# Kernel tuning notes

Hardware: AMD Instinct MI355X
Metric: run time of the kernel (lower is better)

Reference implementation:

```python
import jax, jax.numpy as jnp
import numpy as np

D_MODEL = 2048
N_HEADS = 16
HEAD_DIM = D_MODEL // N_HEADS
LN_EPS = 1e-6  # flax.linen.LayerNorm default
NEG_INF = float('-inf')


def _layernorm_scale_only(x, scale):
    # flax LayerNorm with use_bias=False: normalize over last axis, scale only
    mean = jnp.mean(x, axis=-1, keepdims=True)
    var = jnp.var(x, axis=-1, keepdims=True)
    return (x - mean) * jax.lax.rsqrt(var + LN_EPS) * scale


def setup_inputs() -> dict:
    key = jax.random.key(0)
    ks = jax.random.split(key, 4)
    B, S = 2, 2048
    x = jax.random.normal(ks[0], (B, S, D_MODEL), dtype=jnp.float32)
    Wqkv = jax.random.normal(ks[1], (D_MODEL, 3 * D_MODEL), dtype=jnp.float32) * 0.02
    q_ln_scale = jnp.ones((D_MODEL,), dtype=jnp.float32)
    k_ln_scale = jnp.ones((D_MODEL,), dtype=jnp.float32)
    out_W = jax.random.normal(ks[2], (D_MODEL, D_MODEL), dtype=jnp.float32) * 0.02
    return {"x": x, "Wqkv": Wqkv, "q_ln_scale": q_ln_scale,
            "k_ln_scale": k_ln_scale, "out_W": out_W}


def reference(x, Wqkv, q_ln_scale, k_ln_scale, out_W):
    B, S, _ = x.shape
    qkv = jnp.einsum('bsd,de->bse', x, Wqkv)  # [B,S,3*D] (no bias)
    q, k, v = jnp.split(qkv, 3, axis=-1)
    # QK LayerNorm (attn_qk_ln=True, no bias)
    q = _layernorm_scale_only(q, q_ln_scale)
    k = _layernorm_scale_only(k, k_ln_scale)
    # split heads: [B,S,H,Dh]
    q = q.reshape(B, S, N_HEADS, HEAD_DIM)
    k = k.reshape(B, S, N_HEADS, HEAD_DIM)
    v = v.reshape(B, S, N_HEADS, HEAD_DIM)
    # scaled scores [B,H,S,S]
    scores = jnp.einsum('bshd,bthd->bhst', q / jnp.sqrt(jnp.float32(HEAD_DIM)), k)
    # causal mask: triu(ones, k=1) marks strictly-future positions -> -inf
    causal = jnp.triu(jnp.ones((S, S), dtype=bool), 1)
    scores = jnp.where(causal, NEG_INF, scores)
    # kv-cache mask: arange(S) < S - past_position - S = 0 -> all False (no-op
    # with past_position=0 and no layer_past), faithfully omitted.
    attn = jax.nn.softmax(scores, axis=-1)
    ctx = jnp.einsum('bhst,bthd->bshd', attn, v)  # [B,S,H,Dh]
    out = jnp.einsum('bsd,de->bse', ctx.reshape(B, S, D_MODEL), out_W)
    return out
```

## Files before the change

kernel.cpp:

```cpp
#include <hip/hip_runtime.h>


typedef float f32x4 __attribute__((ext_vector_type(4)));
typedef short s16x8 __attribute__((ext_vector_type(8)));
typedef short s16x4 __attribute__((ext_vector_type(4)));

static __device__ __forceinline__ unsigned short f2bf(float f) {
  unsigned u = __builtin_bit_cast(unsigned, f);
  unsigned r = u + 0x7fffu + ((u >> 16) & 1u);
  return (unsigned short)(r >> 16);
}
static __device__ __forceinline__ float bf2f(unsigned short s) {
  unsigned u = ((unsigned)s) << 16;
  return __builtin_bit_cast(float, u);
}

static __device__ __forceinline__ void gload_lds16(const unsigned short* g, unsigned short* l) {
  __builtin_amdgcn_global_load_lds((const __attribute__((address_space(1))) void*)g,
                                   (__attribute__((address_space(3))) void*)l, 16, 0, 0);
}

__global__ __launch_bounds__(256) void k_cvt4(const float4* __restrict__ in,
                                              s16x4* __restrict__ out, int n) {
  int i = blockIdx.x * 256 + threadIdx.x;
  if (i >= n) return;
  float4 v = in[i];
  s16x4 o = { (short)f2bf(v.x), (short)f2bf(v.y), (short)f2bf(v.z), (short)f2bf(v.w) };
  out[i] = o;
}

__global__ __launch_bounds__(256) void k_twT(const float* __restrict__ in,
                                             unsigned short* __restrict__ out,
                                             int K, int N) {
  __shared__ float tile[32][33];
  const int n0 = blockIdx.x * 32, k0 = blockIdx.y * 32;
  const int tx = threadIdx.x & 31, ty = threadIdx.x >> 5;
#pragma unroll
  for (int rr = 0; rr < 4; ++rr) {
    int kr = ty + rr * 8;
    tile[kr][tx] = in[(size_t)(k0 + kr) * N + n0 + tx];
  }
  __syncthreads();
#pragma unroll
  for (int rr = 0; rr < 4; ++rr) {
    int nr = ty + rr * 8;
    out[(size_t)(n0 + nr) * K + k0 + tx] = f2bf(tile[tx][nr]);
  }
}

template <int BF16OUT>
__global__ __launch_bounds__(512, 2) void k_g3b(const unsigned short* __restrict__ A,
                                                const unsigned short* __restrict__ Bt,
                                                void* __restrict__ Cout,
                                                int N, int K, int npx) {
  __shared__ unsigned short sA[3 * 128 * 64];
  __shared__ unsigned short sB[3 * 256 * 64];
  const int t = threadIdx.x;
  const int wid = t >> 6, lane = t & 63, g = lane >> 4, l15 = lane & 15;
  const int wm2 = wid >> 2, wn2 = wid & 3;
  const int xr = l15 & 7;

  const int xcd = (int)blockIdx.x & 7, idx = (int)blockIdx.x >> 3;
  const int m0 = (idx / npx) * 128;
  const int n0 = (xcd * npx + idx % npx) * 256;

  const int srow = t >> 3;
  const int sslot = (t & 7) ^ (srow & 7);
  const unsigned short* pA = A  + (size_t)(m0 + srow) * K + sslot * 8;
  const unsigned short* pB = Bt + (size_t)(n0 + srow) * K + sslot * 8;

  auto stage = [&](int kt, int buf) {
#pragma unroll
    for (int j = 0; j < 2; ++j)
      gload_lds16(pA + (size_t)(j * 64) * K + kt * 64,
                  sA + buf * 8192 + j * 4096 + t * 8);
#pragma unroll
    for (int j = 0; j < 4; ++j)
      gload_lds16(pB + (size_t)(j * 64) * K + kt * 64,
                  sB + buf * 16384 + j * 4096 + t * 8);
  };

  const int sl0 = (g ^ xr) * 8, sl1 = ((4 + g) ^ xr) * 8;
  const int arow = wm2 * 64 + l15;
  const int brow = wn2 * 32 + l15;

  f32x4 acc[2][4][2];
#pragma unroll
  for (int h = 0; h < 2; ++h)
#pragma unroll
    for (int fm = 0; fm < 4; ++fm)
#pragma unroll
      for (int fn = 0; fn < 2; ++fn) acc[h][fm][fn] = (f32x4){0.f, 0.f, 0.f, 0.f};

  const int NK = K >> 6;
  stage(0, 0);
  stage(1, 1);
  int b0 = 0, b1 = 1, b2 = 2;

  for (int s = 0; s < NK; ++s) {
    if (s + 2 < NK) stage(s + 2, b2);

    if (s + 2 < NK)      asm volatile("s_waitcnt vmcnt(12)" ::: "memory");
    else if (s + 1 < NK) asm volatile("s_waitcnt vmcnt(6)" ::: "memory");
    else                 asm volatile("s_waitcnt vmcnt(0)" ::: "memory");
    __builtin_amdgcn_sched_barrier(0);
    __builtin_amdgcn_s_barrier();
    __builtin_amdgcn_sched_barrier(0);

    const unsigned short* aT = sA + b0 * 8192;
    const unsigned short* bT = sB + b0 * 16384;
    s16x8 af[4][2], bfr[2][2][2];
#pragma unroll
    for (int fm = 0; fm < 4; ++fm) {
      af[fm][0] = *(const s16x8*)&aT[(arow + fm * 16) * 64 + sl0];
      af[fm][1] = *(const s16x8*)&aT[(arow + fm * 16) * 64 + sl1];
    }
#pragma unroll
    for (int h = 0; h < 2; ++h)
#pragma unroll
      for (int fn = 0; fn < 2; ++fn) {
        bfr[h][fn][0] = *(const s16x8*)&bT[(h * 128 + brow + fn * 16) * 64 + sl0];
        bfr[h][fn][1] = *(const s16x8*)&bT[(h * 128 + brow + fn * 16) * 64 + sl1];
      }

    __builtin_amdgcn_s_setprio(1);
#pragma unroll
    for (int fm = 0; fm < 4; ++fm)
#pragma unroll
      for (int h = 0; h < 2; ++h)
#pragma unroll
        for (int fn = 0; fn < 2; ++fn)
#pragma unroll
          for (int ks = 0; ks < 2; ++ks)
            acc[h][fm][fn] = __builtin_amdgcn_mfma_f32_16x16x32_bf16(
                af[fm][ks], bfr[h][fn][ks], acc[h][fm][fn], 0, 0, 0);
    __builtin_amdgcn_s_setprio(0);

    __builtin_amdgcn_sched_barrier(0);
    __builtin_amdgcn_s_barrier();

    int tmp = b0; b0 = b1; b1 = b2; b2 = tmp;
  }

#pragma unroll
  for (int h = 0; h < 2; ++h)
#pragma unroll
    for (int fm = 0; fm < 4; ++fm)
#pragma unroll
      for (int fn = 0; fn < 2; ++fn)
#pragma unroll
        for (int r = 0; r < 4; ++r) {
          const int row = m0 + wm2 * 64 + fm * 16 + g * 4 + r;
          const int col = n0 + h * 128 + wn2 * 32 + fn * 16 + l15;
          if (BF16OUT)
            ((unsigned short*)Cout)[(size_t)row * N + col] = f2bf(acc[h][fm][fn][r]);
          else
            ((float*)Cout)[(size_t)row * N + col] = acc[h][fm][fn][r];
        }
}

__global__ __launch_bounds__(256) void k_ln(unsigned short* __restrict__ qkv,
                                            const float* __restrict__ qsc,
                                            const float* __restrict__ ksc) {
  __shared__ float red[8];
  const int t = threadIdx.x;
  const int w = t >> 6;
  unsigned short* base = qkv + (size_t)blockIdx.x * 6144;
#pragma unroll
  for (int part = 0; part < 2; ++part) {
    unsigned short* p = base + part * 2048 + t * 8;
    s16x8 v = *(const s16x8*)p;
    float f[8], s = 0.f, q = 0.f;
#pragma unroll
    for (int j = 0; j < 8; j++) { f[j] = bf2f((unsigned short)v[j]); s += f[j]; q += f[j] * f[j]; }
#pragma unroll
    for (int m = 1; m < 64; m <<= 1) { s += __shfl_xor(s, m); q += __shfl_xor(q, m); }
    __syncthreads();
    if ((t & 63) == 0) { red[w] = s; red[4 + w] = q; }
    __syncthreads();
    s = red[0] + red[1] + red[2] + red[3];
    q = red[4] + red[5] + red[6] + red[7];
    float mean = s * (1.f / 2048.f);
    float var = q * (1.f / 2048.f) - mean * mean;
    float inv = rsqrtf(var + 1e-6f);
    const float* sc = part ? ksc : qsc;
    float extra = part ? 1.0f : 0.12751743f;
    s16x8 o;
#pragma unroll
    for (int j = 0; j < 8; j++) o[j] = (short)f2bf((f[j] - mean) * inv * (sc[t * 8 + j] * extra));
    *(s16x8*)p = o;
  }
}

__global__ __launch_bounds__(256) void k_vT(const unsigned short* __restrict__ qkv,
                                            unsigned short* __restrict__ vt) {
  __shared__ unsigned short tl[64][136];
  const int bh = blockIdx.y;
  const int b = bh >> 4, h = bh & 15;
  const int s0 = blockIdx.x * 64;
  const int t = threadIdx.x;
#pragma unroll
  for (int it = 0; it < 4; ++it) {
    int flat = it * 256 + t;
    int r = flat >> 4, c = flat & 15;
    s16x8 v = *(const s16x8*)(qkv + (size_t)(b * 2048 + s0 + r) * 6144 + 4096 + h * 128 + c * 8);
    *((s16x8*)&tl[r][c * 8]) = v;
  }
  __syncthreads();
#pragma unroll
  for (int it = 0; it < 4; ++it) {
    int flat = it * 256 + t;
    int d = flat >> 3, cs = flat & 7;
    s16x8 o;
#pragma unroll
    for (int e = 0; e < 8; e++) {
      int key = (cs >> 2) * 32 + (e >> 2) * 16 + (cs & 3) * 4 + (e & 3);
      o[e] = (short)tl[key][d];
    }
    *(s16x8*)(vt + (size_t)(bh * 128 + d) * 2048 + s0 + cs * 8) = o;
  }
}

__global__ __launch_bounds__(256) void k_attn(const unsigned short* __restrict__ qkv,
                                              const unsigned short* __restrict__ vt,
                                              unsigned short* __restrict__ ctx) {
  __shared__ unsigned short sK[2][64 * 128];
  __shared__ unsigned short sV[2][128 * 64];
  const int t = threadIdx.x;
  const int w = t >> 6, lane = t & 63, g = lane >> 4, l15 = lane & 15;
  const int pair = blockIdx.x, h = blockIdx.y, b = blockIdx.z;
  const int qt0 = 31 - pair, qt1 = pair;
  const int n0 = qt0 + 1;
  const int NT = 33;
  const unsigned short* kbase = qkv + (size_t)(b * 2048) * 6144 + 2048 + h * 128;
  const unsigned short* vbase = vt + (size_t)((b * 16 + h) * 128) * 2048;

  auto issue_kv = [&](int k0, int bufi) {
#pragma unroll
    for (int it2 = 0; it2 < 4; ++it2) {
      int flat = it2 * 256 + t;
      int r = flat >> 4, c = flat & 15;
      gload_lds16(kbase + (size_t)(k0 + r) * 6144 + ((c ^ (r & 15)) * 8),
                  (unsigned short*)&sK[bufi][(it2 * 256 + w * 64) * 8]);
    }
#pragma unroll
    for (int it2 = 0; it2 < 4; ++it2) {
      int flat = it2 * 256 + t;
      int d = flat >> 3, z = flat & 7;
      gload_lds16(vbase + (size_t)d * 2048 + k0 + ((z ^ (d & 7)) * 8),
                  (unsigned short*)&sV[bufi][(it2 * 256 + w * 64) * 8]);
    }
  };

  s16x8 bq[4];
  auto load_q = [&](int q0) {
#pragma unroll
    for (int ks = 0; ks < 4; ++ks)
      bq[ks] = *(const s16x8*)(qkv + (size_t)(b * 2048 + q0 + w * 16 + l15) * 6144 +
                               h * 128 + (ks * 4 + g) * 8);
  };

  f32x4 o[8];
  float mrun, lrun;
  auto reset_state = [&]() {
#pragma unroll
    for (int nd = 0; nd < 8; ++nd) o[nd] = (f32x4){0.f, 0.f, 0.f, 0.f};
    mrun = -INFINITY; lrun = 0.f;
  };
  auto write_o = [&](int q0) {
    float ivr[4];
#pragma unroll
    for (int r = 0; r < 4; ++r) ivr[r] = 1.0f / __shfl(lrun, 4 * g + r);
#pragma unroll
    for (int nd = 0; nd < 8; ++nd) {
      const int col = h * 128 + nd * 16 + l15;
#pragma unroll
      for (int r = 0; r < 4; ++r) {
        const int row = b * 2048 + q0 + w * 16 + 4 * g + r;
        ctx[(size_t)row * 2048 + col] = f2bf(o[nd][r] * ivr[r]);
      }
    }
  };

  reset_state();
  load_q(qt0 * 64);
  issue_kv(0, 0);
  int cur = 0;

  for (int it = 0; it < NT; ++it) {
    const int seg = (it < n0) ? 0 : 1;
    const int qt = seg ? qt1 : qt0;
    const int kt = seg ? it - n0 : it;

    if (it + 1 < NT) {
      const int kn = (it + 1 < n0) ? it + 1 : it + 1 - n0;
      issue_kv(kn * 64, cur ^ 1);
      asm volatile("s_waitcnt vmcnt(8)" ::: "memory");
    } else {
      asm volatile("s_waitcnt vmcnt(0)" ::: "memory");
    }
    __builtin_amdgcn_sched_barrier(0);
    __builtin_amdgcn_s_barrier();

    if (seg == 1 && kt == 0) {
      write_o(qt0 * 64);
      reset_state();
      load_q(qt1 * 64);
    }

    const unsigned short* sKc = &sK[cur][0];
    const unsigned short* sVc = &sV[cur][0];

    f32x4 st[4];
#pragma unroll
    for (int mi = 0; mi < 4; ++mi) st[mi] = (f32x4){0.f, 0.f, 0.f, 0.f};
#pragma unroll
    for (int mi = 0; mi < 4; ++mi) {
#pragma unroll
      for (int ks = 0; ks < 4; ++ks) {
        s16x8 ak = *(const s16x8*)&sKc[(mi * 16 + l15) * 128 + (((ks * 4 + g) ^ l15) * 8)];
        st[mi] = __builtin_amdgcn_mfma_f32_16x16x32_bf16(ak, bq[ks], st[mi], 0, 0, 0);
      }
    }

    if (kt == qt) {
      const int qloc = w * 16 + l15;
#pragma unroll
      for (int mi = 0; mi < 4; ++mi)
#pragma unroll
        for (int r = 0; r < 4; ++r)
          if (mi * 16 + 4 * g + r > qloc) st[mi][r] = -INFINITY;
    }

    float mt = -INFINITY;
#pragma unroll
    for (int mi = 0; mi < 4; ++mi)
#pragma unroll
      for (int r = 0; r < 4; ++r) mt = fmaxf(mt, st[mi][r]);
    mt = fmaxf(mt, __shfl_xor(mt, 16));
    mt = fmaxf(mt, __shfl_xor(mt, 32));

    if (!__all(mt <= mrun + 8.f)) {
      const float mnew = fmaxf(mrun, mt);
      const float alpha = exp2f(mrun - mnew);
      lrun *= alpha;
      float ar[4];
#pragma unroll
      for (int r = 0; r < 4; ++r) ar[r] = __shfl(alpha, 4 * g + r);
#pragma unroll
      for (int nd = 0; nd < 8; ++nd)
#pragma unroll
        for (int r = 0; r < 4; ++r) o[nd][r] *= ar[r];
      mrun = mnew;
    }

    float ls = 0.f;
#pragma unroll
    for (int mi = 0; mi < 4; ++mi)
#pragma unroll
      for (int r = 0; r < 4; ++r) {
        float pp = exp2f(st[mi][r] - mrun);
        st[mi][r] = pp;
        ls += pp;
      }
    ls += __shfl_xor(ls, 16);
    ls += __shfl_xor(ls, 32);
    lrun += ls;

    s16x8 pa01, pa23;
#pragma unroll
    for (int j = 0; j < 8; ++j) {
      pa01[j] = (short)f2bf(st[j >> 2][j & 3]);
      pa23[j] = (short)f2bf(st[2 + (j >> 2)][j & 3]);
    }

#pragma unroll
    for (int nd = 0; nd < 8; ++nd) {
      const int d = nd * 16 + l15;
      const int zs = d & 7;
      s16x8 bv0 = *(const s16x8*)&sVc[d * 64 + ((g ^ zs) * 8)];
      s16x8 bv1 = *(const s16x8*)&sVc[d * 64 + (((4 + g) ^ zs) * 8)];
      o[nd] = __builtin_amdgcn_mfma_f32_16x16x32_bf16(pa01, bv0, o[nd], 0, 0, 0);
      o[nd] = __builtin_amdgcn_mfma_f32_16x16x32_bf16(pa23, bv1, o[nd], 0, 0, 0);
    }

    __builtin_amdgcn_sched_barrier(0);
    __builtin_amdgcn_s_barrier();
    cur ^= 1;
  }
  write_o(qt1 * 64);
}

extern "C" void kernel_launch(void* const* d_in, const int* in_sizes, int n_in,
                              void* d_out, int out_size, void* d_ws, size_t ws_size,
                              hipStream_t stream) {
  (void)in_sizes; (void)n_in; (void)out_size; (void)ws_size;
  const float* x    = (const float*)d_in[0];
  const float* Wqkv = (const float*)d_in[1];
  const float* qsc  = (const float*)d_in[2];
  const float* ksc  = (const float*)d_in[3];
  const float* outW = (const float*)d_in[4];

  char* ws = (char*)d_ws;
  unsigned short* xb  = (unsigned short*)(ws);
  unsigned short* wT  = (unsigned short*)(ws + 16777216);
  unsigned short* owT = (unsigned short*)(ws + 41943040);
  unsigned short* qkv = (unsigned short*)(ws + 50331648);
  unsigned short* vt  = (unsigned short*)(ws + 100663296);
  unsigned short* ctx = xb;

  k_cvt4<<<8192, 256, 0, stream>>>((const float4*)x, (s16x4*)xb, 2097152);
  k_twT<<<dim3(192, 64), 256, 0, stream>>>(Wqkv, wT, 2048, 6144);
  k_twT<<<dim3(64, 64), 256, 0, stream>>>(outW, owT, 2048, 2048);
  k_g3b<1><<<768, 512, 0, stream>>>(xb, wT, qkv, 6144, 2048, 3);
  k_ln<<<4096, 256, 0, stream>>>(qkv, qsc, ksc);
  k_vT<<<dim3(32, 32), 256, 0, stream>>>(qkv, vt);
  k_attn<<<dim3(16, 16, 2), 256, 0, stream>>>(qkv, vt, ctx);
  k_g3b<0><<<256, 512, 0, stream>>>(ctx, owT, d_out, 2048, 2048, 1);
}
```

Measured before the change: 306.5 us.

## Replace 512-thread triple-buffered GEMM with 256-thread double-buffered K=32 GEMM

```diff
diff --git a/kernel.cpp b/kernel.cpp
--- a/kernel.cpp
+++ b/kernel.cpp
@@ -48,115 +48,98 @@
   }
 }
 
-template <int BF16OUT>
-__global__ __launch_bounds__(512, 2) void k_g3b(const unsigned short* __restrict__ A,
-                                                const unsigned short* __restrict__ Bt,
-                                                void* __restrict__ Cout,
-                                                int N, int K, int npx) {
-  __shared__ unsigned short sA[3 * 128 * 64];
-  __shared__ unsigned short sB[3 * 256 * 64];
+template <int BF16OUT, int NFN, int MINW>
+__global__ __launch_bounds__(256, MINW) void k_gw(const unsigned short* __restrict__ A,
+                                                  const unsigned short* __restrict__ Bt,
+                                                  void* __restrict__ Cout,
+                                                  int N, int K, int npx) {
+  __shared__ unsigned short sA[2 * 128 * 32];
+  __shared__ unsigned short sB[2 * NFN * 32 * 32];
   const int t = threadIdx.x;
   const int wid = t >> 6, lane = t & 63, g = lane >> 4, l15 = lane & 15;
-  const int wm2 = wid >> 2, wn2 = wid & 3;
-  const int xr = l15 & 7;
+  const int wm = wid >> 1, wn = wid & 1;
 
   const int xcd = (int)blockIdx.x & 7, idx = (int)blockIdx.x >> 3;
   const int m0 = (idx / npx) * 128;
-  const int n0 = (xcd * npx + idx % npx) * 256;
-
-  const int srow = t >> 3;
-  const int sslot = (t & 7) ^ (srow & 7);
-  const unsigned short* pA = A  + (size_t)(m0 + srow) * K + sslot * 8;
-  const unsigned short* pB = Bt + (size_t)(n0 + srow) * K + sslot * 8;
+  const int n0 = (xcd * npx + idx % npx) * (NFN * 32);
+
+  const int u = (t & 7) ^ ((t >> 3) & 7);
+  const int srow = 2 * (t >> 3) + (u >> 2);
+  const int sk = (u & 3) * 8;
+  const unsigned short* pA = A  + (size_t)(m0 + srow) * K + sk;
+  const unsigned short* pB = Bt + (size_t)(n0 + srow) * K + sk;
 
   auto stage = [&](int kt, int buf) {
 #pragma unroll
     for (int j = 0; j < 2; ++j)
-      gload_lds16(pA + (size_t)(j * 64) * K + kt * 64,
-                  sA + buf * 8192 + j * 4096 + t * 8);
-#pragma unroll
-    for (int j = 0; j < 4; ++j)
-      gload_lds16(pB + (size_t)(j * 64) * K + kt * 64,
-                  sB + buf * 16384 + j * 4096 + t * 8);
+      gload_lds16(pA + (size_t)(j * 64) * K + kt * 32,
+                  sA + buf * 4096 + j * 2048 + t * 8);
+#pragma unroll
+    for (int j = 0; j < NFN / 2; ++j)
+      gload_lds16(pB + (size_t)(j * 64) * K + kt * 32,
+                  sB + buf * (NFN * 1024) + j * 2048 + t * 8);
   };
 
-  const int sl0 = (g ^ xr) * 8, sl1 = ((4 + g) ^ xr) * 8;
-  const int arow = wm2 * 64 + l15;
-  const int brow = wn2 * 32 + l15;
-
-  f32x4 acc[2][4][2];
-#pragma unroll
-  for (int h = 0; h < 2; ++h)
-#pragma unroll
-    for (int fm = 0; fm < 4; ++fm)
-#pragma unroll
-      for (int fn = 0; fn < 2; ++fn) acc[h][fm][fn] = (f32x4){0.f, 0.f, 0.f, 0.f};
-
-  const int NK = K >> 6;
-  stage(0, 0);
-  stage(1, 1);
-  int b0 = 0, b1 = 1, b2 = 2;
+  const int si = (((l15 & 1) * 4 + g) ^ ((l15 >> 1) & 7));
+  const int baseA = (wm * 32 + (l15 >> 1)) * 64 + si * 8;
+  const int baseB = (wn * NFN * 8 + (l15 >> 1)) * 64 + si * 8;
+
+  f32x4 acc[4][NFN];
+#pragma unroll
+  for (int fm = 0; fm < 4; ++fm)
+#pragma unroll
+    for (int fn = 0; fn < NFN; ++fn) acc[fm][fn] = (f32x4){0.f, 0.f, 0.f, 0.f};
+
+  const int NK = K >> 5;
+  stage(0, 0); stage(1, 1);
+  if constexpr (NFN == 8) asm volatile("s_waitcnt vmcnt(6)" ::: "memory");
+  else                    asm volatile("s_waitcnt vmcnt(4)" ::: "memory");
+  __builtin_amdgcn_sched_barrier(0);
+  __builtin_amdgcn_s_barrier();
 
   for (int s = 0; s < NK; ++s) {
-    if (s + 2 < NK) stage(s + 2, b2);
-
-    if (s + 2 < NK)      asm volatile("s_waitcnt vmcnt(12)" ::: "memory");
-    else if (s + 1 < NK) asm volatile("s_waitcnt vmcnt(6)" ::: "memory");
-    else                 asm volatile("s_waitcnt vmcnt(0)" ::: "memory");
+    const unsigned short* aT = sA + (s & 1) * 4096;
+    const unsigned short* bT = sB + (s & 1) * (NFN * 1024);
+
+    s16x8 af[4];
+#pragma unroll
+    for (int fm = 0; fm < 4; ++fm) af[fm] = *(const s16x8*)&aT[baseA + fm * 512];
+    __builtin_amdgcn_s_setprio(1);
+#pragma unroll
+    for (int fn = 0; fn < NFN; ++fn) {
+      s16x8 bf = *(const s16x8*)&bT[baseB + fn * 512];
+#pragma unroll
+      for (int fm = 0; fm < 4; ++fm)
+        acc[fm][fn] = __builtin_amdgcn_mfma_f32_16x16x32_bf16(af[fm], bf, acc[fm][fn], 0, 0, 0);
+    }
+    __builtin_amdgcn_s_setprio(0);
+
     __builtin_amdgcn_sched_barrier(0);
     __builtin_amdgcn_s_barrier();
-    __builtin_amdgcn_sched_barrier(0);
-
-    const unsigned short* aT = sA + b0 * 8192;
-    const unsigned short* bT = sB + b0 * 16384;
-    s16x8 af[4][2], bfr[2][2][2];
-#pragma unroll
-    for (int fm = 0; fm < 4; ++fm) {
-      af[fm][0] = *(const s16x8*)&aT[(arow + fm * 16) * 64 + sl0];
-      af[fm][1] = *(const s16x8*)&aT[(arow + fm * 16) * 64 + sl1];
-    }
-#pragma unroll
-    for (int h = 0; h < 2; ++h)
-#pragma unroll
-      for (int fn = 0; fn < 2; ++fn) {
-        bfr[h][fn][0] = *(const s16x8*)&bT[(h * 128 + brow + fn * 16) * 64 + sl0];
-        bfr[h][fn][1] = *(const s16x8*)&bT[(h * 128 + brow + fn * 16) * 64 + sl1];
-      }
-
-    __builtin_amdgcn_s_setprio(1);
-#pragma unroll
-    for (int fm = 0; fm < 4; ++fm)
-#pragma unroll
-      for (int h = 0; h < 2; ++h)
-#pragma unroll
-        for (int fn = 0; fn < 2; ++fn)
-#pragma unroll
-          for (int ks = 0; ks < 2; ++ks)
-            acc[h][fm][fn] = __builtin_amdgcn_mfma_f32_16x16x32_bf16(
-                af[fm][ks], bfr[h][fn][ks], acc[h][fm][fn], 0, 0, 0);
-    __builtin_amdgcn_s_setprio(0);
-
+    if (s + 2 < NK) {
+      stage(s + 2, s & 1);
+      if constexpr (NFN == 8) asm volatile("s_waitcnt vmcnt(6)" ::: "memory");
+      else                    asm volatile("s_waitcnt vmcnt(4)" ::: "memory");
+    } else if (s + 1 < NK) {
+      asm volatile("s_waitcnt vmcnt(0)" ::: "memory");
+    }
     __builtin_amdgcn_sched_barrier(0);
     __builtin_amdgcn_s_barrier();
-
-    int tmp = b0; b0 = b1; b1 = b2; b2 = tmp;
-  }
-
-#pragma unroll
-  for (int h = 0; h < 2; ++h)
-#pragma unroll
-    for (int fm = 0; fm < 4; ++fm)
-#pragma unroll
-      for (int fn = 0; fn < 2; ++fn)
-#pragma unroll
-        for (int r = 0; r < 4; ++r) {
-          const int row = m0 + wm2 * 64 + fm * 16 + g * 4 + r;
-          const int col = n0 + h * 128 + wn2 * 32 + fn * 16 + l15;
-          if (BF16OUT)
-            ((unsigned short*)Cout)[(size_t)row * N + col] = f2bf(acc[h][fm][fn][r]);
-          else
-            ((float*)Cout)[(size_t)row * N + col] = acc[h][fm][fn][r];
-        }
+  }
+
+#pragma unroll
+  for (int fm = 0; fm < 4; ++fm)
+#pragma unroll
+    for (int fn = 0; fn < NFN; ++fn)
+#pragma unroll
+      for (int r = 0; r < 4; ++r) {
+        const int row = m0 + wm * 64 + fm * 16 + g * 4 + r;
+        const int col = n0 + wn * (NFN * 16) + fn * 16 + l15;
+        if (BF16OUT)
+          ((unsigned short*)Cout)[(size_t)row * N + col] = f2bf(acc[fm][fn][r]);
+        else
+          ((float*)Cout)[(size_t)row * N + col] = acc[fm][fn][r];
+      }
 }
 
 __global__ __launch_bounds__(256) void k_ln(unsigned short* __restrict__ qkv,
@@ -412,9 +395,9 @@
   k_cvt4<<<8192, 256, 0, stream>>>((const float4*)x, (s16x4*)xb, 2097152);
   k_twT<<<dim3(192, 64), 256, 0, stream>>>(Wqkv, wT, 2048, 6144);
   k_twT<<<dim3(64, 64), 256, 0, stream>>>(outW, owT, 2048, 2048);
-  k_g3b<1><<<768, 512, 0, stream>>>(xb, wT, qkv, 6144, 2048, 3);
+  k_gw<1, 8, 3><<<768, 256, 0, stream>>>(xb, wT, qkv, 6144, 2048, 3);
   k_ln<<<4096, 256, 0, stream>>>(qkv, qsc, ksc);
   k_vT<<<dim3(32, 32), 256, 0, stream>>>(qkv, vt);
   k_attn<<<dim3(16, 16, 2), 256, 0, stream>>>(qkv, vt, ctx);
-  k_g3b<0><<<256, 512, 0, stream>>>(ctx, owT, d_out, 2048, 2048, 1);
-}
+  k_gw<0, 4, 2><<<512, 256, 0, stream>>>(ctx, owT, d_out, 2048, 2048, 2);
+}
```

New measurement: 281.4 us. -8.2%, faster.
